# Kernel optimization log

Hardware: AMD Instinct MI355X
Metric: run time of the kernel (lower is better)

The kernel has to match this reference:

```python
import jax, jax.numpy as jnp
import numpy as np

TOP_K = 2
SCALING = 32.0 / 64.0  # lora_alpha / reservoir_size


def setup_inputs() -> dict:
    key = jax.random.key(0)
    ks = jax.random.split(key, 6)
    Bsz, S, Din, Dout, R, E = 4, 2048, 4096, 4096, 64, 16
    x = jax.random.normal(ks[0], (Bsz, S, Din), dtype=jnp.float32)
    base_w = jax.random.normal(ks[1], (Dout, Din), dtype=jnp.float32) * 0.02
    base_b = jax.random.normal(ks[2], (Dout,), dtype=jnp.float32) * 0.02
    A = jax.random.normal(ks[3], (R, Din), dtype=jnp.float32) * (1.0 / np.sqrt(Din))
    B = jax.random.normal(ks[4], (E, Dout, R), dtype=jnp.float32) * 0.02
    router_w = jax.random.normal(ks[5], (E, Din), dtype=jnp.float32) * 0.02
    return {"x": x, "base_w": base_w, "base_b": base_b, "A": A, "B": B, "router_w": router_w}


def reference(x, base_w, base_b, A, B, router_w):
    # base linear: [b,s,din] @ [dout,din]^T + bias
    base_out = jnp.einsum('bsi,oi->bso', x, base_w) + base_b
    # low-rank projection through fixed reservoir A (activation=identity, dropout off)
    res_hidden = jnp.einsum('bsi,ri->bsr', x, A)          # [b,s,r]
    # routing
    logits = jnp.einsum('bsi,ei->bse', x, router_w)       # [b,s,E]
    probs = jax.nn.softmax(logits, axis=-1)
    topw, topi = jax.lax.top_k(probs, TOP_K)              # [b,s,k]
    topw = topw / (jnp.sum(topw, axis=-1, keepdims=True) + 1e-6)
    num_experts = B.shape[0]
    # combine weights per expert: sum_k w_k * onehot(idx_k)  -> [b,s,E]
    combine = jnp.sum(jax.nn.one_hot(topi, num_experts, dtype=x.dtype) * topw[..., None], axis=-2)
    # weighted per-expert lowrank B matmul and combine
    delta = jnp.einsum('bse,bsr,eor->bso', combine, res_hidden, B)
    return base_out + delta * SCALING
```

## Files before the change

kernel.cpp:

```cpp
#include <hip/hip_runtime.h>
#include <cstdint>
#include <cstddef>

typedef short short8 __attribute__((ext_vector_type(8)));
typedef float f32x4 __attribute__((ext_vector_type(4)));

#define DIN  4096
#define DOUT 4096
#define RANK 64
#define NEXP 16
#define NTOK 8192
#define KCAT 5120

__device__ __forceinline__ unsigned short f2bf(float f) {
    unsigned int u = __builtin_bit_cast(unsigned int, f);
    u = (u + 0x7FFFu + ((u >> 16) & 1u)) >> 16;
    return (unsigned short)u;
}
__device__ __forceinline__ void async_cp16(const void* g, void* lds) {
    __builtin_amdgcn_global_load_lds(
        (const __attribute__((address_space(1))) void*)g,
        (__attribute__((address_space(3))) void*)lds, 16, 0, 0);
}

__global__ void __launch_bounds__(256) prep_all_kernel(
        const float* __restrict__ x, const float* __restrict__ rw,
        const float* __restrict__ bw, const float* __restrict__ Bm,
        const float* __restrict__ Am,
        unsigned short* __restrict__ Xcat, unsigned short* __restrict__ Wcat,
        unsigned short* __restrict__ W1A, float* __restrict__ Lg) {
    __shared__ __align__(16) float xsl[8][532];
    __shared__ __align__(16) float red[8][16][16];
    const int tid = threadIdx.x;

    if (blockIdx.x < 1024) {
        const int t0 = blockIdx.x * 8;
        const int tt = tid >> 5, l32 = tid & 31;
        const int eg = tid >> 6, ts = (tid >> 4) & 3, cc = tid & 15;
        float part[2][4] = {};

        for (int w = 0; w < 8; ++w) {
            #pragma unroll
            for (int sub = 0; sub < 4; ++sub) {
                const int col = w * 512 + sub * 128 + l32 * 4;
                const float4 xv = *(const float4*)&x[(size_t)(t0 + tt) * DIN + col];
                unsigned short b0 = f2bf(xv.x), b1 = f2bf(xv.y),
                               b2 = f2bf(xv.z), b3 = f2bf(xv.w);
                uint2 pk = { (unsigned)b0 | ((unsigned)b1 << 16),
                             (unsigned)b2 | ((unsigned)b3 << 16) };
                *(uint2*)&Xcat[(size_t)(t0 + tt) * KCAT + col] = pk;
                *(float4*)&xsl[tt][sub * 128 + l32 * 4] = xv;
            }
            __syncthreads();
            #pragma unroll
            for (int j = 0; j < 8; ++j) {
                const int colb = w * 512 + (j * 16 + cc) * 4;
                const float4 r0 = *(const float4*)&rw[(size_t)(eg * 4 + 0) * DIN + colb];
                const float4 r1 = *(const float4*)&rw[(size_t)(eg * 4 + 1) * DIN + colb];
                const float4 r2 = *(const float4*)&rw[(size_t)(eg * 4 + 2) * DIN + colb];
                const float4 r3 = *(const float4*)&rw[(size_t)(eg * 4 + 3) * DIN + colb];
                #pragma unroll
                for (int t2 = 0; t2 < 2; ++t2) {
                    const int t = ts * 2 + t2;
                    const float4 xv = *(const float4*)&xsl[t][(j * 16 + cc) * 4];
                    part[t2][0] += xv.x * r0.x + xv.y * r0.y + xv.z * r0.z + xv.w * r0.w;
                    part[t2][1] += xv.x * r1.x + xv.y * r1.y + xv.z * r1.z + xv.w * r1.w;
                    part[t2][2] += xv.x * r2.x + xv.y * r2.y + xv.z * r2.z + xv.w * r2.w;
                    part[t2][3] += xv.x * r3.x + xv.y * r3.y + xv.z * r3.z + xv.w * r3.w;
                }
            }
            __syncthreads();
        }
        #pragma unroll
        for (int t2 = 0; t2 < 2; ++t2)
            #pragma unroll
            for (int e = 0; e < 4; ++e)
                red[ts * 2 + t2][eg * 4 + e][cc] = part[t2][e];
        __syncthreads();
        if (tid < 128) {
            const int t = tid >> 4, e = tid & 15;
            float s = 0.f;
            #pragma unroll
            for (int c = 0; c < 16; ++c) s += red[t][e][c];
            Lg[(size_t)(t0 + t) * NEXP + e] = s;
        }
    } else {
        const unsigned NG1 = (unsigned)DOUT * KCAT / 8u;
        const unsigned NGT = NG1 + 64u * DIN / 8u;
        for (unsigned g = (blockIdx.x - 1024) * 256u + tid; g < NGT;
             g += 2048u * 256u) {
            const float* src;
            unsigned short* dst;
            if (g < NG1) {
                unsigned o  = g / 640u;
                unsigned c8 = (g - o * 640u) * 8u;
                dst = Wcat + (size_t)o * KCAT + c8;
                if (c8 < DIN) {
                    src = bw + (size_t)o * DIN + c8;
                } else {
                    unsigned cc2 = c8 - DIN;
                    unsigned e = cc2 >> 6, r = cc2 & 63u;
                    src = Bm + ((size_t)e * DOUT + o) * RANK + r;
                }
            } else {
                unsigned g2 = g - NG1;
                unsigned row = g2 >> 9;
                unsigned c8  = (g2 & 511u) * 8u;
                dst = W1A + (size_t)row * DIN + c8;
                src = Am + (size_t)row * DIN + c8;
            }
            float4 v0 = *(const float4*)(src);
            float4 v1 = *(const float4*)(src + 4);
            uint4 pk;
            pk.x = (unsigned)f2bf(v0.x) | ((unsigned)f2bf(v0.y) << 16);
            pk.y = (unsigned)f2bf(v0.z) | ((unsigned)f2bf(v0.w) << 16);
            pk.z = (unsigned)f2bf(v1.x) | ((unsigned)f2bf(v1.y) << 16);
            pk.w = (unsigned)f2bf(v1.z) | ((unsigned)f2bf(v1.w) << 16);
            *(uint4*)dst = pk;
        }
    }
}

__global__ void __launch_bounds__(256) proj_moe_kernel(
        const unsigned short* __restrict__ Xcat,
        const unsigned short* __restrict__ W1A,
        const float* __restrict__ Lg, unsigned short* __restrict__ XcatW) {
    __shared__ __align__(16) unsigned short Xs[32 * 64];
    __shared__ __align__(16) unsigned short Ws[64 * 64];
    __shared__ __align__(16) float cw[32][16];
    __shared__ __align__(16) float hbuf[32][68];
    const int tid = threadIdx.x;
    const int wave = tid >> 6, lane = tid & 63;
    const int quad = lane >> 4, l16 = lane & 15;
    const int t0 = blockIdx.x * 32;
    const int srow = tid >> 3;
    const int scol = ((tid & 7) ^ (srow & 7)) * 8;

    if (tid < 32) {
        float l[16];
        #pragma unroll
        for (int e = 0; e < 16; ++e) l[e] = Lg[(size_t)(t0 + tid) * NEXP + e];
        int i1 = 0; float b1v = l[0];
        #pragma unroll
        for (int e = 1; e < 16; ++e) if (l[e] > b1v) { b1v = l[e]; i1 = e; }
        int i2 = -1; float b2v = -1e30f;
        #pragma unroll
        for (int e = 0; e < 16; ++e) if (e != i1 && l[e] > b2v) { b2v = l[e]; i2 = e; }
        float S = 0.f;
        #pragma unroll
        for (int e = 0; e < 16; ++e) S += expf(l[e] - b1v);
        const float p1 = 1.0f / S;
        const float p2 = expf(b2v - b1v) / S;
        const float d = p1 + p2 + 1e-6f;
        const float c1 = 0.5f * p1 / d;
        const float c2 = 0.5f * p2 / d;
        #pragma unroll
        for (int e = 0; e < 16; ++e)
            cw[tid][e] = (e == i1) ? c1 : (e == i2) ? c2 : 0.0f;
    }

    f32x4 acc[2] = {};
    for (int kt = 0; kt < DIN / 64; ++kt) {
        const int k0 = kt * 64;
        async_cp16(Xcat + (size_t)(t0 + srow) * KCAT + k0 + scol,
                   (char*)Xs + wave * 1024);
        #pragma unroll
        for (int i = 0; i < 2; ++i)
            async_cp16(W1A + (size_t)(i * 32 + srow) * DIN + k0 + scol,
                       (char*)Ws + i * 4096 + wave * 1024);
        __syncthreads();
        #pragma unroll
        for (int kk = 0; kk < 2; ++kk) {
            const int cs = ((kk * 4 + quad) ^ (l16 & 7)) << 3;
            short8 bn = *(const short8*)&Ws[(wave * 16 + l16) * 64 + cs];
            #pragma unroll
            for (int i = 0; i < 2; ++i) {
                short8 am = *(const short8*)&Xs[(i * 16 + l16) * 64 + cs];
                acc[i] = __builtin_amdgcn_mfma_f32_16x16x32_bf16(am, bn, acc[i], 0, 0, 0);
            }
        }
        __syncthreads();
    }
    #pragma unroll
    for (int i = 0; i < 2; ++i)
        #pragma unroll
        for (int r = 0; r < 4; ++r)
            hbuf[i * 16 + quad * 4 + r][wave * 16 + l16] = acc[i][r];
    __syncthreads();
    const int t = tid >> 3, part = tid & 7;
    unsigned short* dst = XcatW + (size_t)(t0 + t) * KCAT + DIN;
    #pragma unroll
    for (int ee = 0; ee < 2; ++ee) {
        const int e = part * 2 + ee;
        const float c = cw[t][e];
        #pragma unroll
        for (int r8 = 0; r8 < 8; ++r8) {
            uint4 pk;
            unsigned short o16[8];
            #pragma unroll
            for (int k = 0; k < 8; ++k)
                o16[k] = f2bf(c * hbuf[t][r8 * 8 + k]);
            pk.x = (unsigned)o16[0] | ((unsigned)o16[1] << 16);
            pk.y = (unsigned)o16[2] | ((unsigned)o16[3] << 16);
            pk.z = (unsigned)o16[4] | ((unsigned)o16[5] << 16);
            pk.w = (unsigned)o16[6] | ((unsigned)o16[7] << 16);
            *(uint4*)(dst + e * 64 + r8 * 8) = pk;
        }
    }
}

__global__ void __launch_bounds__(256) gemm_main_kernel(
        const unsigned short* __restrict__ Xcat,
        const unsigned short* __restrict__ Wcat,
        const float* __restrict__ bias, float* __restrict__ out) {
    __shared__ __align__(16) unsigned short Xs[128 * 64];
    __shared__ __align__(16) unsigned short Ws[128 * 64];
    const int tid = threadIdx.x;
    const int wave = tid >> 6, lane = tid & 63;
    const int quad = lane >> 4, l16 = lane & 15;
    const int bn0 = blockIdx.x * 128;
    const int bm0 = blockIdx.y * 128;
    const int srow = tid >> 3;
    const int scol = ((tid & 7) ^ (srow & 7)) * 8;
    const unsigned short* gx = Xcat + (size_t)(bm0 + srow) * KCAT + scol;
    const unsigned short* gw = Wcat + (size_t)(bn0 + srow) * KCAT + scol;
    const int wm0 = (wave & 1) * 64;
    const int wn0 = (wave >> 1) * 64;
    f32x4 acc[4][4] = {};
    for (int kt = 0; kt < KCAT / 64; ++kt) {
        const int k0 = kt * 64;
        #pragma unroll
        for (int i = 0; i < 4; ++i) {
            async_cp16(gx + (size_t)(i * 32) * KCAT + k0, (char*)Xs + i * 4096 + wave * 1024);
            async_cp16(gw + (size_t)(i * 32) * KCAT + k0, (char*)Ws + i * 4096 + wave * 1024);
        }
        __syncthreads();
        #pragma unroll
        for (int kk = 0; kk < 2; ++kk) {
            short8 am[4], bn[4];
            #pragma unroll
            for (int i = 0; i < 4; ++i)
                am[i] = *(const short8*)&Xs[(wm0 + i * 16 + l16) * 64 +
                                            (((kk * 4 + quad) ^ (l16 & 7)) << 3)];
            #pragma unroll
            for (int j = 0; j < 4; ++j)
                bn[j] = *(const short8*)&Ws[(wn0 + j * 16 + l16) * 64 +
                                            (((kk * 4 + quad) ^ (l16 & 7)) << 3)];
            #pragma unroll
            for (int i = 0; i < 4; ++i)
                #pragma unroll
                for (int j = 0; j < 4; ++j)
                    acc[i][j] = __builtin_amdgcn_mfma_f32_16x16x32_bf16(
                        am[i], bn[j], acc[i][j], 0, 0, 0);
        }
        __syncthreads();
    }
    #pragma unroll
    for (int j = 0; j < 4; ++j) {
        const int col = bn0 + wn0 + j * 16 + l16;
        const float bj = bias[col];
        #pragma unroll
        for (int i = 0; i < 4; ++i) {
            const int row0 = bm0 + wm0 + i * 16 + quad * 4;
            #pragma unroll
            for (int r = 0; r < 4; ++r)
                out[(size_t)(row0 + r) * DOUT + col] = acc[i][j][r] + bj;
        }
    }
}

extern "C" void kernel_launch(void* const* d_in, const int* in_sizes, int n_in,
                              void* d_out, int out_size, void* d_ws, size_t ws_size,
                              hipStream_t stream) {
    const float* x  = (const float*)d_in[0];
    const float* bw = (const float*)d_in[1];
    const float* bb = (const float*)d_in[2];
    const float* Am = (const float*)d_in[3];
    const float* Bm = (const float*)d_in[4];
    const float* rw = (const float*)d_in[5];
    float* out = (float*)d_out;
    char* ws = (char*)d_ws;
    unsigned short* Xcat = (unsigned short*)(ws);
    unsigned short* Wcat = (unsigned short*)(ws + 83886080);
    unsigned short* W1A  = (unsigned short*)(ws + 125829120);
    float* Lg = (float*)(ws + 126353408);

    hipLaunchKernelGGL(prep_all_kernel, dim3(3072),   dim3(256), 0, stream,
                       x, rw, bw, Bm, Am, Xcat, Wcat, W1A, Lg);
    hipLaunchKernelGGL(proj_moe_kernel, dim3(256),    dim3(256), 0, stream,
                       Xcat, W1A, Lg, Xcat);
    hipLaunchKernelGGL(gemm_main_kernel, dim3(32, 64), dim3(256), 0, stream,
                       Xcat, Wcat, bb, out);
}
```

Before: 750.1 us.

## Use 32x32x16 MFMA in main GEMM and halve proj_moe token tile

The main GEMM switches from 16x16x32 to 32x32x16 bf16 MFMA tiles, so each wave issues 4 larger MFMAs per k-step with fewer LDS fragment loads per FLOP. The epilogue is remapped to the 32x32 accumulator layout. Separately, proj_moe_kernel now handles 16 tokens per block with 128-wide K tiles, doubling the grid to 512 blocks to raise parallelism on the many-CU device. The swizzled LDS indexing is rewritten for the new shapes, which risks bank conflicts or indexing errors.

```diff
diff --git a/kernel.cpp b/kernel.cpp
--- a/kernel.cpp
+++ b/kernel.cpp
@@ -4,6 +4,7 @@
 
 typedef short short8 __attribute__((ext_vector_type(8)));
 typedef float f32x4 __attribute__((ext_vector_type(4)));
+typedef float f32x16 __attribute__((ext_vector_type(16)));
 
 #define DIN  4096
 #define DOUT 4096
@@ -125,18 +126,19 @@
         const unsigned short* __restrict__ Xcat,
         const unsigned short* __restrict__ W1A,
         const float* __restrict__ Lg, unsigned short* __restrict__ XcatW) {
-    __shared__ __align__(16) unsigned short Xs[32 * 64];
-    __shared__ __align__(16) unsigned short Ws[64 * 64];
-    __shared__ __align__(16) float cw[32][16];
-    __shared__ __align__(16) float hbuf[32][68];
+    __shared__ __align__(16) unsigned short Xs[16 * 128];
+    __shared__ __align__(16) unsigned short Ws[64 * 128];
+    __shared__ __align__(16) float cw[16][16];
+    __shared__ __align__(16) float hbuf[16][68];
     const int tid = threadIdx.x;
     const int wave = tid >> 6, lane = tid & 63;
     const int quad = lane >> 4, l16 = lane & 15;
-    const int t0 = blockIdx.x * 32;
-    const int srow = tid >> 3;
-    const int scol = ((tid & 7) ^ (srow & 7)) * 8;
-
-    if (tid < 32) {
+    const int t0 = blockIdx.x * 16;
+
+    const int rX = tid >> 4, cXs = tid & 15;
+    const int cX = (cXs & 8) | ((cXs ^ rX) & 7);
+
+    if (tid < 16) {
         float l[16];
         #pragma unroll
         for (int e = 0; e < 16; ++e) l[e] = Lg[(size_t)(t0 + tid) * NEXP + e];
@@ -159,53 +161,51 @@
             cw[tid][e] = (e == i1) ? c1 : (e == i2) ? c2 : 0.0f;
     }
 
-    f32x4 acc[2] = {};
-    for (int kt = 0; kt < DIN / 64; ++kt) {
-        const int k0 = kt * 64;
-        async_cp16(Xcat + (size_t)(t0 + srow) * KCAT + k0 + scol,
+    f32x4 acc = {};
+    for (int kt = 0; kt < DIN / 128; ++kt) {
+        const int k0 = kt * 128;
+        async_cp16(Xcat + (size_t)(t0 + rX) * KCAT + k0 + cX * 8,
                    (char*)Xs + wave * 1024);
         #pragma unroll
-        for (int i = 0; i < 2; ++i)
-            async_cp16(W1A + (size_t)(i * 32 + srow) * DIN + k0 + scol,
+        for (int i = 0; i < 4; ++i) {
+            const int s = i * 256 + tid;
+            const int rW = s >> 4, cWs = s & 15;
+            const int cWc = (cWs & 8) | ((cWs ^ rW) & 7);
+            async_cp16(W1A + (size_t)rW * DIN + k0 + cWc * 8,
                        (char*)Ws + i * 4096 + wave * 1024);
-        __syncthreads();
-        #pragma unroll
-        for (int kk = 0; kk < 2; ++kk) {
-            const int cs = ((kk * 4 + quad) ^ (l16 & 7)) << 3;
-            short8 bn = *(const short8*)&Ws[(wave * 16 + l16) * 64 + cs];
-            #pragma unroll
-            for (int i = 0; i < 2; ++i) {
-                short8 am = *(const short8*)&Xs[(i * 16 + l16) * 64 + cs];
-                acc[i] = __builtin_amdgcn_mfma_f32_16x16x32_bf16(am, bn, acc[i], 0, 0, 0);
-            }
+        }
+        __syncthreads();
+        #pragma unroll
+        for (int kk = 0; kk < 4; ++kk) {
+            const int c = kk * 4 + quad;
+            const int sa = ((c & 8) | ((c ^ l16) & 7)) << 3;
+            const int rb = wave * 16 + l16;
+            const int sb = ((c & 8) | ((c ^ rb) & 7)) << 3;
+            short8 am = *(const short8*)&Xs[l16 * 128 + sa];
+            short8 bn = *(const short8*)&Ws[rb * 128 + sb];
+            acc = __builtin_amdgcn_mfma_f32_16x16x32_bf16(am, bn, acc, 0, 0, 0);
         }
         __syncthreads();
     }
     #pragma unroll
-    for (int i = 0; i < 2; ++i)
-        #pragma unroll
-        for (int r = 0; r < 4; ++r)
-            hbuf[i * 16 + quad * 4 + r][wave * 16 + l16] = acc[i][r];
+    for (int r = 0; r < 4; ++r)
+        hbuf[quad * 4 + r][wave * 16 + l16] = acc[r];
     __syncthreads();
-    const int t = tid >> 3, part = tid & 7;
-    unsigned short* dst = XcatW + (size_t)(t0 + t) * KCAT + DIN;
+    const int t = tid >> 4, e = tid & 15;
+    const float c = cw[t][e];
+    unsigned short* dst = XcatW + (size_t)(t0 + t) * KCAT + DIN + e * 64;
     #pragma unroll
-    for (int ee = 0; ee < 2; ++ee) {
-        const int e = part * 2 + ee;
-        const float c = cw[t][e];
-        #pragma unroll
-        for (int r8 = 0; r8 < 8; ++r8) {
-            uint4 pk;
-            unsigned short o16[8];
-            #pragma unroll
-            for (int k = 0; k < 8; ++k)
-                o16[k] = f2bf(c * hbuf[t][r8 * 8 + k]);
-            pk.x = (unsigned)o16[0] | ((unsigned)o16[1] << 16);
-            pk.y = (unsigned)o16[2] | ((unsigned)o16[3] << 16);
-            pk.z = (unsigned)o16[4] | ((unsigned)o16[5] << 16);
-            pk.w = (unsigned)o16[6] | ((unsigned)o16[7] << 16);
-            *(uint4*)(dst + e * 64 + r8 * 8) = pk;
-        }
+    for (int r8 = 0; r8 < 8; ++r8) {
+        unsigned short o16[8];
+        #pragma unroll
+        for (int k = 0; k < 8; ++k)
+            o16[k] = f2bf(c * hbuf[t][r8 * 8 + k]);
+        uint4 pk;
+        pk.x = (unsigned)o16[0] | ((unsigned)o16[1] << 16);
+        pk.y = (unsigned)o16[2] | ((unsigned)o16[3] << 16);
+        pk.z = (unsigned)o16[4] | ((unsigned)o16[5] << 16);
+        pk.w = (unsigned)o16[6] | ((unsigned)o16[7] << 16);
+        *(uint4*)(dst + r8 * 8) = pk;
     }
 }
 
@@ -217,7 +217,7 @@
     __shared__ __align__(16) unsigned short Ws[128 * 64];
     const int tid = threadIdx.x;
     const int wave = tid >> 6, lane = tid & 63;
-    const int quad = lane >> 4, l16 = lane & 15;
+    const int half = lane >> 5, l32 = lane & 31;
     const int bn0 = blockIdx.x * 128;
     const int bm0 = blockIdx.y * 128;
     const int srow = tid >> 3;
@@ -226,7 +226,7 @@
     const unsigned short* gw = Wcat + (size_t)(bn0 + srow) * KCAT + scol;
     const int wm0 = (wave & 1) * 64;
     const int wn0 = (wave >> 1) * 64;
-    f32x4 acc[4][4] = {};
+    f32x16 acc[2][2] = {};
     for (int kt = 0; kt < KCAT / 64; ++kt) {
         const int k0 = kt * 64;
         #pragma unroll
@@ -236,35 +236,40 @@
         }
         __syncthreads();
         #pragma unroll
-        for (int kk = 0; kk < 2; ++kk) {
-            short8 am[4], bn[4];
-            #pragma unroll
-            for (int i = 0; i < 4; ++i)
-                am[i] = *(const short8*)&Xs[(wm0 + i * 16 + l16) * 64 +
-                                            (((kk * 4 + quad) ^ (l16 & 7)) << 3)];
-            #pragma unroll
-            for (int j = 0; j < 4; ++j)
-                bn[j] = *(const short8*)&Ws[(wn0 + j * 16 + l16) * 64 +
-                                            (((kk * 4 + quad) ^ (l16 & 7)) << 3)];
-            #pragma unroll
-            for (int i = 0; i < 4; ++i)
+        for (int kk2 = 0; kk2 < 4; ++kk2) {
+            const int c = kk2 * 2 + half;
+            short8 am[2], bn[2];
+            #pragma unroll
+            for (int i = 0; i < 2; ++i) {
+                const int r = wm0 + i * 32 + l32;
+                am[i] = *(const short8*)&Xs[r * 64 + ((c ^ (r & 7)) << 3)];
+            }
+            #pragma unroll
+            for (int j = 0; j < 2; ++j) {
+                const int r = wn0 + j * 32 + l32;
+                bn[j] = *(const short8*)&Ws[r * 64 + ((c ^ (r & 7)) << 3)];
+            }
+            #pragma unroll
+            for (int i = 0; i < 2; ++i)
                 #pragma unroll
-                for (int j = 0; j < 4; ++j)
-                    acc[i][j] = __builtin_amdgcn_mfma_f32_16x16x32_bf16(
+                for (int j = 0; j < 2; ++j)
+                    acc[i][j] = __builtin_amdgcn_mfma_f32_32x32x16_bf16(
                         am[i], bn[j], acc[i][j], 0, 0, 0);
         }
         __syncthreads();
     }
     #pragma unroll
-    for (int j = 0; j < 4; ++j) {
-        const int col = bn0 + wn0 + j * 16 + l16;
+    for (int j = 0; j < 2; ++j) {
+        const int col = bn0 + wn0 + j * 32 + l32;
         const float bj = bias[col];
         #pragma unroll
-        for (int i = 0; i < 4; ++i) {
-            const int row0 = bm0 + wm0 + i * 16 + quad * 4;
-            #pragma unroll
-            for (int r = 0; r < 4; ++r)
-                out[(size_t)(row0 + r) * DOUT + col] = acc[i][j][r] + bj;
+        for (int i = 0; i < 2; ++i) {
+            const int rb = bm0 + wm0 + i * 32 + 4 * half;
+            #pragma unroll
+            for (int r = 0; r < 16; ++r) {
+                const int row = rb + (r & 3) + 8 * (r >> 2);
+                out[(size_t)row * DOUT + col] = acc[i][j][r] + bj;
+            }
         }
     }
 }
@@ -287,7 +292,7 @@
 
     hipLaunchKernelGGL(prep_all_kernel, dim3(3072),   dim3(256), 0, stream,
                        x, rw, bw, Bm, Am, Xcat, Wcat, W1A, Lg);
-    hipLaunchKernelGGL(proj_moe_kernel, dim3(256),    dim3(256), 0, stream,
+    hipLaunchKernelGGL(proj_moe_kernel, dim3(512),    dim3(256), 0, stream,
                        Xcat, W1A, Lg, Xcat);
     hipLaunchKernelGGL(gemm_main_kernel, dim3(32, 64), dim3(256), 0, stream,
                        Xcat, Wcat, bb, out);
```

After: 688.4 us. 1.09x faster.
